# Kernel tuning notes

Measured on AMD Instinct MI355X. Metric: run time of the kernel, lower is better.

## Reference

```python
import jax, jax.numpy as jnp
import numpy as np

SAMPLE = 16          # init kwarg `sample`
DILATED_RATE = 2     # init kwarg `dilated_rate`
RADIUS = 16.0        # hardcoded in forward: ball_query(16, ...)
NSAMPLE = SAMPLE * DILATED_RATE
XYZ_SCALE = 30.0     # spread points so radius-16 ball is a real neighborhood


def setup_inputs() -> dict:
    key = jax.random.key(0)
    k1, k2 = jax.random.split(key)
    xyz = jax.random.normal(k1, (4, 4096, 3), dtype=jnp.float32) * XYZ_SCALE
    feature = jax.random.normal(k2, (4, 4096, 64), dtype=jnp.float32)
    return {"xyz": xyz, "feature": feature}


def _ball_query(xyz, radius, nsample):
    """pointnet2-style ball query: for each point, the first `nsample` point
    indices (in ascending index order) with squared distance < radius^2;
    rows with fewer than nsample hits are padded with the first hit.
    xyz: [B,N,3] -> idx int32 [B,N,nsample]."""
    B, N, _ = xyz.shape
    sq = jnp.sum(xyz * xyz, axis=-1)                                   # [B,N]
    d2 = sq[:, :, None] + sq[:, None, :] - 2.0 * jnp.einsum(
        'bnd,bmd->bnm', xyz, xyz)                                      # [B,N,N]
    in_ball = d2 < (radius * radius)
    # score = N - j for in-ball points, 0 otherwise; top_k then returns the
    # smallest in-ball indices j, already sorted ascending in j.
    col_score = (N - jnp.arange(N, dtype=jnp.int32))[None, None, :]
    score = jnp.where(in_ball, col_score, 0)                           # [B,N,N]
    vals, idx = jax.lax.top_k(score, nsample)                          # [B,N,K]
    first = idx[..., 0:1]
    return jnp.where(vals > 0, idx, first)                             # pad with first hit


def _group(points, idx):
    """grouping_operation: points [B,N,C] (channel-last), idx [B,N,K] ->
    grouped [B,C,N,K]."""
    gathered = jax.vmap(lambda p, i: p[i])(points, idx)  # [B,N,K,C]
    return gathered.transpose(0, 3, 1, 2)                # [B,C,N,K]


def reference(xyz, feature):
    ids = _ball_query(xyz, RADIUS, NSAMPLE)              # [B,N,NSAMPLE]
    center = ids[:, :, 0:1]
    if DILATED_RATE == 1:
        dilated_ids = ids[:, :, :SAMPLE]
    else:
        region = ids[:, :, (DILATED_RATE - 1) * SAMPLE: DILATED_RATE * SAMPLE - 1]
        dilated_ids = jnp.concatenate([center, region], axis=-1)  # [B,N,SAMPLE]
    dilated_xyz = _group(xyz, dilated_ids)          # [B,3,N,SAMPLE]
    dilated_feature = _group(feature, dilated_ids)  # [B,C,N,SAMPLE]
    return (dilated_xyz, dilated_feature)
```

## Files before the change

kernel.cpp:

```cpp
#include <hip/hip_runtime.h>


#define BB 4
#define NN 4096
#define KK 16
#define PLANE (NN * KK)

__global__ __launch_bounds__(256)
void build_soa(const float* __restrict__ xyz, float4* __restrict__ P)
{
#pragma clang fp contract(off)
    const int g = blockIdx.x * 256 + threadIdx.x;
    const float x = xyz[3 * g], y = xyz[3 * g + 1], z = xyz[3 * g + 2];
    const float sq = (x * x + y * y) + z * z;
    P[g] = make_float4(x, y, z, sq);
}

__global__ __launch_bounds__(256, 4)
void query_gather(const float4* __restrict__ P, const float* __restrict__ feat,
                  float* __restrict__ out)
{
#pragma clang fp contract(off)
    __shared__ int sids[4 * KK];

    const int beta = blockIdx.x;
    const int b    = beta >> 10;
    const int p0   = (beta & 1023) * 4;
    const int t    = threadIdx.x;
    const int lane = t & 63;
    const int wave = t >> 6;

    const float4* Pb = P + (b << 12);

    {
        const int   pl  = wave;
        const float4 pi = Pb[p0 + pl];
        const float sqi = pi.w;
        const unsigned long long lt = (1ULL << lane) - 1ULL;
        int fj  = 0x7fffffff;
        int cnt = 0;
        int* row = sids + pl * KK;

        float4 a = Pb[lane];
        float4 c = Pb[64 + lane];
        for (int jc = 0; jc < NN / 64; jc += 2) {
            float4 na, nc;
            if (jc + 2 < NN / 64) {
                na = Pb[((jc + 2) << 6) + lane];
                nc = Pb[((jc + 3) << 6) + lane];
            }
            const int j0 = (jc << 6) + lane;
            const int j1 = j0 + 64;
            const float dot0 = (pi.x * a.x + pi.y * a.y) + pi.z * a.z;
            const float d20  = (sqi + a.w) - 2.0f * dot0;
            const float dot1 = (pi.x * c.x + pi.y * c.y) + pi.z * c.z;
            const float d21  = (sqi + c.w) - 2.0f * dot1;
            const bool h0 = d20 < 256.0f;
            const bool h1 = d21 < 256.0f;
            const unsigned long long m0 = __ballot(h0);
            const unsigned long long m1 = __ballot(h1);
            if (m0 | m1) {
                if (fj == 0x7fffffff) { if (h0) fj = j0; else if (h1) fj = j1; }
                const int r0 = cnt + __popcll(m0 & lt);
                if (h0 && r0 >= 16 && r0 <= 30) row[r0 - 15] = j0;
                cnt += __popcll(m0);
                const int r1 = cnt + __popcll(m1 & lt);
                if (h1 && r1 >= 16 && r1 <= 30) row[r1 - 15] = j1;
                cnt += __popcll(m1);
                if (cnt >= 31) break;
            }
            a = na; c = nc;
        }

        for (int off = 32; off; off >>= 1) {
            const int o = __shfl_xor(fj, off, 64);
            fj = fj < o ? fj : o;
        }
        const int hi = (cnt < 31 ? cnt : 31) - 16;
        if (lane < KK && (lane == 0 || lane > hi)) row[lane] = fj;
    }
    __syncthreads();

    const int rowi = t & 63;
    const int part = t >> 6;
    const int id   = sids[rowi];
    const int ob   = (beta & 1023) * 64 + rowi;

    if (part == 0) {
        const float4 p = Pb[id];
        float* o0 = out + (size_t)b * 3 * PLANE + ob;
        o0[0]         = p.x;
        o0[PLANE]     = p.y;
        o0[2 * PLANE] = p.z;
    }

    const float4* frow = reinterpret_cast<const float4*>(feat + ((size_t)(b << 12) + id) * 64) + part * 4;
    float* o1 = out + (size_t)BB * 3 * PLANE + (size_t)b * 64 * PLANE
                    + (size_t)(part * 16) * PLANE + ob;
#pragma unroll
    for (int q = 0; q < 4; ++q) {
        const float4 v = frow[q];
        float* oc = o1 + (size_t)(4 * q) * PLANE;
        oc[0]         = v.x;
        oc[PLANE]     = v.y;
        oc[2 * PLANE] = v.z;
        oc[3 * PLANE] = v.w;
    }
}

extern "C" void kernel_launch(void* const* d_in, const int* in_sizes, int n_in,
                              void* d_out, int out_size, void* d_ws, size_t ws_size,
                              hipStream_t stream) {
    const float* xyz  = (const float*)d_in[0];
    const float* feat = (const float*)d_in[1];
    float* out = (float*)d_out;

    float4* P = (float4*)d_ws;

    build_soa   <<<BB * NN / 256, 256, 0, stream>>>(xyz, P);
    query_gather<<<BB * NN / 4,   256, 0, stream>>>(P, feat, out);
}
```

Measured before the change: 115.1 us.

## Replace brute-force ball query with uniform-grid cell binning and bitmask ranking

Points are binned into a 20^3 uniform grid with cell size equal to the radius. This uses a counting pass, a prefix-scan kernel and a scatter kernel that writes cell-sorted points and their original indices. Each query wave then scans only the 27 neighbouring cells and sets in-ball indices in a shared bitmask. A wave-wide prefix popcount over that bitmask recovers the ascending-index ranks, so the brute-force scan over all N points is no longer needed. The cost is three extra launches plus a memset, global and LDS atomics, and edge-cell clamping that can crowd outlier points into border cells.

```diff
diff --git a/kernel.cpp b/kernel.cpp
--- a/kernel.cpp
+++ b/kernel.cpp
@@ -5,22 +5,85 @@
 #define NN 4096
 #define KK 16
 #define PLANE (NN * KK)
+#define NC 20
+#define NCELLS (NC * NC * NC)
+
+__device__ __forceinline__ int cell1d(float v)
+{
+    int c = (int)floorf((v + 160.0f) * 0.0625f);
+    c = c < 0 ? 0 : c;
+    return c > (NC - 1) ? (NC - 1) : c;
+}
 
 __global__ __launch_bounds__(256)
-void build_soa(const float* __restrict__ xyz, float4* __restrict__ P)
+void build_soa(const float* __restrict__ xyz, float4* __restrict__ P,
+               int* __restrict__ counts)
 {
 #pragma clang fp contract(off)
     const int g = blockIdx.x * 256 + threadIdx.x;
     const float x = xyz[3 * g], y = xyz[3 * g + 1], z = xyz[3 * g + 2];
     const float sq = (x * x + y * y) + z * z;
     P[g] = make_float4(x, y, z, sq);
+    const int c = (cell1d(z) * NC + cell1d(y)) * NC + cell1d(x);
+    atomicAdd(&counts[(g >> 12) * NCELLS + c], 1);
+}
+
+__global__ __launch_bounds__(256)
+void scan_cells(int* __restrict__ counts, int* __restrict__ cellStart)
+{
+    const int b = blockIdx.x;
+    int* cnt = counts + b * NCELLS;
+    int* cs  = cellStart + b * (NCELLS + 1);
+    const int t = threadIdx.x;
+    const int lane = t & 63, wave = t >> 6;
+
+    const int c0 = t * 32;
+    const int c1 = (c0 + 32 < NCELLS) ? c0 + 32 : NCELLS;
+    int s = 0;
+    for (int c = c0; c < c1; ++c) s += cnt[c];
+
+    int x = s;
+#pragma unroll
+    for (int off = 1; off < 64; off <<= 1) {
+        const int u = __shfl_up(x, off, 64);
+        if (lane >= off) x += u;
+    }
+    __shared__ int wsum[4];
+    if (lane == 63) wsum[wave] = x;
+    __syncthreads();
+    int wb = 0;
+    for (int w = 0; w < wave; ++w) wb += wsum[w];
+    int acc = wb + x - s;
+
+    for (int c = c0; c < c1; ++c) {
+        const int v = cnt[c];
+        cs[c]  = acc;
+        cnt[c] = acc;
+        acc += v;
+    }
+    if (t == 0) cs[NCELLS] = NN;
+}
+
+__global__ __launch_bounds__(256)
+void scatter(const float4* __restrict__ P, int* __restrict__ cursor,
+             float4* __restrict__ SP, int* __restrict__ SI)
+{
+    const int g = blockIdx.x * 256 + threadIdx.x;
+    const float4 p = P[g];
+    const int c = (cell1d(p.z) * NC + cell1d(p.y)) * NC + cell1d(p.x);
+    const int b = g >> 12;
+    const int slot = atomicAdd(&cursor[b * NCELLS + c], 1);
+    SP[(b << 12) + slot] = p;
+    SI[(b << 12) + slot] = g & (NN - 1);
 }
 
 __global__ __launch_bounds__(256, 4)
-void query_gather(const float4* __restrict__ P, const float* __restrict__ feat,
-                  float* __restrict__ out)
+void query_gather(const float4* __restrict__ P, const float4* __restrict__ SP,
+                  const int* __restrict__ SI, const int* __restrict__ CS,
+                  const float* __restrict__ feat, float* __restrict__ out)
 {
 #pragma clang fp contract(off)
+    __shared__ unsigned int mask[4][128];
     __shared__ int sids[4 * KK];
 
     const int beta = blockIdx.x;
@@ -30,51 +93,77 @@
     const int lane = t & 63;
     const int wave = t >> 6;
 
-    const float4* Pb = P + (b << 12);
+    ((unsigned int*)mask)[t]       = 0u;
+    ((unsigned int*)mask)[t + 256] = 0u;
+    __syncthreads();
+
+    const float4* Pb  = P  + (b << 12);
+    const float4* Sb  = SP + (b << 12);
+    const int*    Ib  = SI + (b << 12);
+    const int*    csb = CS + b * (NCELLS + 1);
+
+    const float4 pi = Pb[p0 + wave];
 
     {
-        const int   pl  = wave;
-        const float4 pi = Pb[p0 + pl];
         const float sqi = pi.w;
-        const unsigned long long lt = (1ULL << lane) - 1ULL;
-        int fj  = 0x7fffffff;
-        int cnt = 0;
-        int* row = sids + pl * KK;
-
-        float4 a = Pb[lane];
-        float4 c = Pb[64 + lane];
-        for (int jc = 0; jc < NN / 64; jc += 2) {
-            float4 na, nc;
-            if (jc + 2 < NN / 64) {
-                na = Pb[((jc + 2) << 6) + lane];
-                nc = Pb[((jc + 3) << 6) + lane];
+        unsigned int* m = mask[wave];
+        const int cx = cell1d(pi.x), cy = cell1d(pi.y), cz = cell1d(pi.z);
+        const int x0 = cx > 0 ? cx - 1 : 0;
+        const int x1 = cx < NC - 1 ? cx + 1 : NC - 1;
+        const int y0 = cy > 0 ? cy - 1 : 0;
+        const int y1 = cy < NC - 1 ? cy + 1 : NC - 1;
+        const int z0 = cz > 0 ? cz - 1 : 0;
+        const int z1 = cz < NC - 1 ? cz + 1 : NC - 1;
+        for (int zz = z0; zz <= z1; ++zz)
+            for (int yy = y0; yy <= y1; ++yy) {
+                const int cb = (zz * NC + yy) * NC;
+                const int s  = csb[cb + x0];
+                const int e  = csb[cb + x1 + 1];
+                for (int k = s + lane; k < e; k += 64) {
+                    const float4 a = Sb[k];
+                    const float dot = (pi.x * a.x + pi.y * a.y) + pi.z * a.z;
+                    const float d2  = (sqi + a.w) - 2.0f * dot;
+                    if (d2 < 256.0f) {
+                        const int j = Ib[k];
+                        atomicOr(&m[j >> 5], 1u << (j & 31));
+                    }
+                }
             }
-            const int j0 = (jc << 6) + lane;
-            const int j1 = j0 + 64;
-            const float dot0 = (pi.x * a.x + pi.y * a.y) + pi.z * a.z;
-            const float d20  = (sqi + a.w) - 2.0f * dot0;
-            const float dot1 = (pi.x * c.x + pi.y * c.y) + pi.z * c.z;
-            const float d21  = (sqi + c.w) - 2.0f * dot1;
-            const bool h0 = d20 < 256.0f;
-            const bool h1 = d21 < 256.0f;
-            const unsigned long long m0 = __ballot(h0);
-            const unsigned long long m1 = __ballot(h1);
-            if (m0 | m1) {
-                if (fj == 0x7fffffff) { if (h0) fj = j0; else if (h1) fj = j1; }
-                const int r0 = cnt + __popcll(m0 & lt);
-                if (h0 && r0 >= 16 && r0 <= 30) row[r0 - 15] = j0;
-                cnt += __popcll(m0);
-                const int r1 = cnt + __popcll(m1 & lt);
-                if (h1 && r1 >= 16 && r1 <= 30) row[r1 - 15] = j1;
-                cnt += __popcll(m1);
-                if (cnt >= 31) break;
-            }
-            a = na; c = nc;
+    }
+    __syncthreads();
+
+    {
+        const unsigned int* m = mask[wave];
+        const unsigned int lo  = m[2 * lane];
+        const unsigned int hiw = m[2 * lane + 1];
+        const unsigned long long w = ((unsigned long long)hiw << 32) | lo;
+        const int c = __popcll(w);
+        int x = c;
+#pragma unroll
+        for (int off = 1; off < 64; off <<= 1) {
+            const int u = __shfl_up(x, off, 64);
+            if (lane >= off) x += u;
         }
-
+        const int cnt  = __shfl(x, 63, 64);
+        const int base = x - c;
+
+        int fj = 0x7fffffff;
+        if (w) fj = (lane << 6) + __builtin_ctzll(w);
         for (int off = 32; off; off >>= 1) {
             const int o = __shfl_xor(fj, off, 64);
             fj = fj < o ? fj : o;
+        }
+
+        int* row = sids + wave * KK;
+        if (w && base <= 30 && base + c > 16) {
+            unsigned long long ww = w;
+            int r = base;
+            while (ww) {
+                if (r > 30) break;
+                if (r >= 16) row[r - 15] = (lane << 6) + __builtin_ctzll(ww);
+                ww &= ww - 1;
+                ++r;
+            }
         }
         const int hi = (cnt < 31 ? cnt : 31) - 16;
         if (lane < KK && (lane == 0 || lane > hi)) row[lane] = fj;
@@ -115,8 +204,16 @@
     const float* feat = (const float*)d_in[1];
     float* out = (float*)d_out;
 
-    float4* P = (float4*)d_ws;
-
-    build_soa   <<<BB * NN / 256, 256, 0, stream>>>(xyz, P);
-    query_gather<<<BB * NN / 4,   256, 0, stream>>>(P, feat, out);
-}
+    char* ws = (char*)d_ws;
+    float4* P         = (float4*)(ws);
+    float4* SP        = (float4*)(ws + 262144);
+    int*    SI        = (int*)   (ws + 524288);
+    int*    counts    = (int*)   (ws + 589824);
+    int*    cellStart = (int*)   (ws + 720896);
+
+    hipMemsetAsync(counts, 0, BB * NCELLS * sizeof(int), stream);
+    build_soa  <<<BB * NN / 256, 256, 0, stream>>>(xyz, P, counts);
+    scan_cells <<<BB,            256, 0, stream>>>(counts, cellStart);
+    scatter    <<<BB * NN / 256, 256, 0, stream>>>(P, counts, SP, SI);
+    query_gather<<<BB * NN / 4,  256, 0, stream>>>(P, SP, SI, cellStart, feat, out);
+}
```

After: 131.9 us. +14.6%, slower.
